# Kernel optimization log

Hardware: AMD Instinct MI355X
Metric: run time of the kernel (lower is better)

## Reference

```python
import jax, jax.numpy as jnp
import numpy as np

B, L, D_MODEL = 16, 2048, 512
S, D_LLM = 1000, 1024
H, E = 8, 64  # n_heads, d_keys
D_OUT = 64


def setup_inputs() -> dict:
    key = jax.random.key(0)
    ks = jax.random.split(key, 11)
    sc = lambda d: 1.0 / np.sqrt(d)
    return {
        "target_embedding": jax.random.normal(ks[0], (B, L, D_MODEL), dtype=jnp.float32),
        "source_embedding": jax.random.normal(ks[1], (S, D_LLM), dtype=jnp.float32),
        "value_embedding": jax.random.normal(ks[2], (S, D_LLM), dtype=jnp.float32),
        "Wq": jax.random.normal(ks[3], (D_MODEL, H * E), dtype=jnp.float32) * sc(D_MODEL),
        "bq": jnp.zeros((H * E,), dtype=jnp.float32),
        "Wk": jax.random.normal(ks[4], (D_LLM, H * E), dtype=jnp.float32) * sc(D_LLM),
        "bk": jnp.zeros((H * E,), dtype=jnp.float32),
        "Wv": jax.random.normal(ks[5], (D_LLM, H * E), dtype=jnp.float32) * sc(D_LLM),
        "bv": jnp.zeros((H * E,), dtype=jnp.float32),
        "Wo": jax.random.normal(ks[6], (H * E, D_OUT), dtype=jnp.float32) * sc(H * E),
        "bo": jnp.zeros((D_OUT,), dtype=jnp.float32),
    }


def reference(target_embedding, source_embedding, value_embedding,
              Wq, bq, Wk, bk, Wv, bv, Wo, bo):
    # projections
    q = (target_embedding @ Wq + bq).reshape(B, L, H, E)   # blhe
    k = (source_embedding @ Wk + bk).reshape(S, H, E)      # she
    v = (value_embedding @ Wv + bv).reshape(S, H, E)       # she
    scale = 1.0 / jnp.sqrt(jnp.asarray(E, dtype=q.dtype))
    scores = jnp.einsum("blhe,she->bhls", q, k)            # (B,H,L,S)
    A = jax.nn.softmax(scale * scores, axis=-1)            # dropout in eval mode = identity
    out = jnp.einsum("bhls,she->blhe", A, v).reshape(B, L, H * E)
    return out @ Wo + bo                                    # (B,L,64)
```

## Files before the change

### kernel.cpp

```cpp
#include <hip/hip_runtime.h>

typedef __attribute__((ext_vector_type(4))) float  f32x4;
typedef __attribute__((ext_vector_type(8))) __bf16 bf16x8;
typedef __attribute__((ext_vector_type(4))) __bf16 bf16x4;

static __device__ __forceinline__ f32x4 mfma16(bf16x8 a, bf16x8 b, f32x4 c) {
  return __builtin_amdgcn_mfma_f32_16x16x32_bf16(a, b, c, 0, 0, 0);
}

typedef __attribute__((address_space(1))) const unsigned int* gas1_t;
typedef __attribute__((address_space(3))) unsigned int* las3_t;
static __device__ __forceinline__ void glds16(const void* g, void* l) {
  __builtin_amdgcn_global_load_lds((gas1_t)g, (las3_t)l, 16, 0, 0);
}

#define QSCALE 0.18033688011112042f

__global__ __launch_bounds__(256) void prep_wT(
    const float* __restrict__ Wq, const float* __restrict__ Wk,
    const float* __restrict__ Wv, const float* __restrict__ Wo,
    __bf16* __restrict__ wqT, __bf16* __restrict__ wkT,
    __bf16* __restrict__ wvT, __bf16* __restrict__ woT) {
  __shared__ float tile[32][33];
  const int t = blockIdx.x;
  const float* in; __bf16* out; int K, N, tk, tn;
  if (t < 256)       { in = Wq; out = wqT; K = 512;  N = 512; tk = t & 15;          tn = t >> 4; }
  else if (t < 768)  { in = Wk; out = wkT; K = 1024; N = 512; tk = (t-256) & 31;    tn = (t-256) >> 5; }
  else if (t < 1280) { in = Wv; out = wvT; K = 1024; N = 512; tk = (t-768) & 31;    tn = (t-768) >> 5; }
  else               { in = Wo; out = woT; K = 512;  N = 64;  tk = (t-1280) & 15;   tn = (t-1280) >> 4; }
  const int k0 = tk * 32, n0 = tn * 32;
  const int c = threadIdx.x & 31, r = threadIdx.x >> 5;
#pragma unroll
  for (int i = 0; i < 4; ++i)
    tile[r + i * 8][c] = in[(size_t)(k0 + r + i * 8) * N + n0 + c];
  __syncthreads();
#pragma unroll
  for (int i = 0; i < 4; ++i)
    out[(size_t)(n0 + r + i * 8) * K + k0 + c] = (__bf16)tile[c][r + i * 8];
}

__global__ __launch_bounds__(256) void prep_cvt(
    const float* __restrict__ tgt, const float* __restrict__ src,
    const float* __restrict__ val,
    __bf16* __restrict__ tgtb, __bf16* __restrict__ srcb, __bf16* __restrict__ valb) {
  const int j = blockIdx.x * 256 + threadIdx.x;
  const int C0 = 32768 * 512 / 4;
  const int CV = 1024 * 1024 / 4;
  if (j < C0) {
    f32x4 v = *(const f32x4*)&tgt[(size_t)j * 4];
    bf16x4 o; o[0]=(__bf16)v[0]; o[1]=(__bf16)v[1]; o[2]=(__bf16)v[2]; o[3]=(__bf16)v[3];
    *(bf16x4*)&tgtb[(size_t)j * 4] = o;
  } else if (j < C0 + 2 * CV) {
    const int which = (j - C0) / CV;
    const int u = (j - C0) - which * CV;
    const float* in = which ? val : src;
    __bf16* outp = which ? valb : srcb;
    bf16x4 o;
    if (u * 4 < 1000 * 1024) {
      f32x4 v = *(const f32x4*)&in[(size_t)u * 4];
      o[0]=(__bf16)v[0]; o[1]=(__bf16)v[1]; o[2]=(__bf16)v[2]; o[3]=(__bf16)v[3];
    } else {
      o[0]=(__bf16)0.0f; o[1]=(__bf16)0.0f; o[2]=(__bf16)0.0f; o[3]=(__bf16)0.0f;
    }
    *(bf16x4*)&outp[(size_t)u * 4] = o;
  }
}

template <int MODE>
__global__ __launch_bounds__(256, 2) void gemm_bt(
    const __bf16* __restrict__ A, const __bf16* __restrict__ BT,
    const float* __restrict__ bias, float scale,
    __bf16* __restrict__ C, int M, int N, int K) {
  const int n0 = blockIdx.x * 128, m0 = blockIdx.y * 128;
  __shared__ __bf16 sA[128 * 32], sB[128 * 32];
  const int t = threadIdx.x;
  const int w = t >> 6, lane = t & 63;
  const int wr = w >> 1, wc = w & 1;
  const int lr = lane & 15, lg = lane >> 4;

  const int grow = w * 32 + (lane >> 2);
  const int lslot = (lane & 3) ^ ((lane >> 2) & 3) ^ (lane >> 4);
  char* const sAw = (char*)sA + w * 2048;
  char* const sBw = (char*)sB + w * 2048;

  const int rslot = (lg ^ (lr & 3) ^ ((lr >> 2) & 3)) << 4;
  const int aOff = wr * 4096 + lr * 64 + rslot;
  const int bOff = wc * 4096 + lr * 64 + rslot;

  f32x4 acc[4][4];
#pragma unroll
  for (int i = 0; i < 4; ++i)
#pragma unroll
    for (int j = 0; j < 4; ++j) acc[i][j] = f32x4{0.f, 0.f, 0.f, 0.f};

  const size_t gaBase0 = (size_t)(m0 + grow) * K + lslot * 8;
  const size_t gaBase1 = (size_t)(m0 + grow + 16) * K + lslot * 8;
  const size_t gbBase0 = (size_t)(n0 + grow) * K + lslot * 8;
  const size_t gbBase1 = (size_t)(n0 + grow + 16) * K + lslot * 8;

  for (int kc = 0; kc < K; kc += 32) {
    __syncthreads();
    glds16(&A[gaBase0 + kc], sAw);
    glds16(&A[gaBase1 + kc], sAw + 1024);
    glds16(&BT[gbBase0 + kc], sBw);
    glds16(&BT[gbBase1 + kc], sBw + 1024);
    __syncthreads();

    bf16x8 af[4], bfr[4];
#pragma unroll
    for (int i = 0; i < 4; ++i) {
      af[i]  = *(const bf16x8*)((const char*)sA + aOff + i * 1024);
      bfr[i] = *(const bf16x8*)((const char*)sB + bOff + i * 1024);
    }
    __builtin_amdgcn_s_setprio(1);
#pragma unroll
    for (int i = 0; i < 4; ++i)
#pragma unroll
      for (int j = 0; j < 4; ++j) acc[i][j] = mfma16(af[i], bfr[j], acc[i][j]);
    __builtin_amdgcn_s_setprio(0);
  }

#pragma unroll
  for (int i = 0; i < 4; ++i) {
    const int rowb = m0 + wr * 64 + i * 16 + lg * 4;
#pragma unroll
    for (int j = 0; j < 4; ++j) {
      const int col = n0 + wc * 64 + j * 16 + lr;
      const float bb = bias ? bias[col] : 0.0f;
      if (MODE == 0) {
#pragma unroll
        for (int r = 0; r < 4; ++r)
          C[(size_t)(rowb + r) * N + col] = (__bf16)((acc[i][j][r] + bb) * scale);
      } else {
        bf16x4 v;
#pragma unroll
        for (int r = 0; r < 4; ++r) v[r] = (__bf16)((acc[i][j][r] + bb) * scale);
        *(bf16x4*)&C[(size_t)col * M + rowb] = v;
      }
    }
  }
}

__global__ __launch_bounds__(256, 4) void attn_kernel(
    const __bf16* __restrict__ qg, const __bf16* __restrict__ kg,
    const __bf16* __restrict__ vtg, __bf16* __restrict__ og) {
  const int bid = blockIdx.x;
  const int lt = bid & 15, h = (bid >> 4) & 7, b = bid >> 7;
  const int w = threadIdx.x >> 6, lane = threadIdx.x & 63;
  const int lr = lane & 15, g = lane >> 4, lr7 = lane & 7;
  const int l0 = lt * 128 + w * 32;

  __shared__ __bf16 sK[2][4096];
  __shared__ __bf16 sV[2][4096];
  __shared__ __bf16 sP[4][1024];
  char* const pbase = (char*)&sP[w][0];

  const int srowi = lane >> 3;
  const int sslot = (lane & 7) ^ srowi;
  const int krow = w * 16 + srowi;
  const size_t kgBase = (size_t)krow * 512 + h * 64 + sslot * 8;
  const size_t vgBase = (size_t)(h * 64 + krow) * 1024 + sslot * 8;

  bf16x8 qf[2][2];
#pragma unroll
  for (int qi = 0; qi < 2; ++qi)
#pragma unroll
    for (int hf = 0; hf < 2; ++hf)
      qf[qi][hf] = *(const bf16x8*)&qg[
          ((size_t)b * 2048 + l0 + qi * 16 + lr) * 512 + h * 64 + hf * 32 + g * 8];

  f32x4 o[2][4], lsacc[2];
#pragma unroll
  for (int qi = 0; qi < 2; ++qi) {
#pragma unroll
    for (int j = 0; j < 4; ++j) o[qi][j] = f32x4{0.f, 0.f, 0.f, 0.f};
    lsacc[qi] = f32x4{0.f, 0.f, 0.f, 0.f};
  }

  bf16x8 ones8;
#pragma unroll
  for (int i = 0; i < 8; ++i) ones8[i] = (__bf16)1.0f;

  const int eOff0 = lr * 128 + ((g ^ lr7) << 4);
  const int pswz = lr7 << 4;

  glds16(&kg[kgBase], (char*)&sK[0][0] + w * 2048);
  glds16(&kg[kgBase + (size_t)8 * 512], (char*)&sK[0][0] + w * 2048 + 1024);
  glds16(&vtg[vgBase], (char*)&sV[0][0] + w * 2048);
  glds16(&vtg[vgBase + (size_t)8 * 1024], (char*)&sV[0][0] + w * 2048 + 1024);
  __syncthreads();

  for (int sc = 0; sc < 16; ++sc) {
    const int p = sc & 1;
    if (sc < 15) {
      const int sn = (sc + 1) * 64;
      char* nk = (char*)&sK[p ^ 1][0] + w * 2048;
      char* nv = (char*)&sV[p ^ 1][0] + w * 2048;
      glds16(&kg[kgBase + (size_t)sn * 512], nk);
      glds16(&kg[kgBase + (size_t)(sn + 8) * 512], nk + 1024);
      glds16(&vtg[vgBase + sn], nv);
      glds16(&vtg[vgBase + sn + 8 * 1024], nv + 1024);
    }
    const char* kbuf = (const char*)&sK[p][0];
    const char* vbuf = (const char*)&sV[p][0];

    bf16x8 kf[4][2];
#pragma unroll
    for (int t = 0; t < 4; ++t) {
      kf[t][0] = *(const bf16x8*)(kbuf + t * 2048 + eOff0);
      kf[t][1] = *(const bf16x8*)(kbuf + t * 2048 + (eOff0 ^ 64));
    }
    f32x4 d[2][4];
    __builtin_amdgcn_s_setprio(1);
#pragma unroll
    for (int qi = 0; qi < 2; ++qi)
#pragma unroll
      for (int t = 0; t < 4; ++t) {
        f32x4 z = {0.f, 0.f, 0.f, 0.f};
        z = mfma16(kf[t][0], qf[qi][0], z);
        z = mfma16(kf[t][1], qf[qi][1], z);
        d[qi][t] = z;
      }
    __builtin_amdgcn_s_setprio(0);
    if (sc == 15) {
#pragma unroll
      for (int qi = 0; qi < 2; ++qi)
#pragma unroll
        for (int t = 0; t < 4; ++t)
#pragma unroll
          for (int r = 0; r < 4; ++r)
            if (960 + t * 16 + 4 * g + r >= 1000) d[qi][t][r] = -1.0e30f;
    }

    bf16x8 vf[2][4];
#pragma unroll
    for (int kc = 0; kc < 2; ++kc)
#pragma unroll
      for (int j = 0; j < 4; ++j)
        vf[kc][j] = *(const bf16x8*)(vbuf + j * 2048 + (eOff0 ^ (kc * 64)));

#pragma unroll
    for (int qi = 0; qi < 2; ++qi) {
#pragma unroll
      for (int t = 0; t < 4; ++t) {
        bf16x4 pv;
        pv[0] = (__bf16)exp2f(d[qi][t][0]);
        pv[1] = (__bf16)exp2f(d[qi][t][1]);
        pv[2] = (__bf16)exp2f(d[qi][t][2]);
        pv[3] = (__bf16)exp2f(d[qi][t][3]);
        *(bf16x4*)(pbase + lr * 128 + ((t * 32 + g * 8) ^ pswz)) = pv;
      }
#pragma unroll
      for (int kc = 0; kc < 2; ++kc) {
        const bf16x8 pB = *(const bf16x8*)(
            pbase + lr * 128 + ((kc * 64 + g * 16) ^ pswz));
        __builtin_amdgcn_s_setprio(1);
        lsacc[qi] = mfma16(ones8, pB, lsacc[qi]);
#pragma unroll
        for (int j = 0; j < 4; ++j)
          o[qi][j] = mfma16(vf[kc][j], pB, o[qi][j]);
        __builtin_amdgcn_s_setprio(0);
      }
    }
    __syncthreads();
  }

#pragma unroll
  for (int qi = 0; qi < 2; ++qi) {
    const float rinv = 1.0f / lsacc[qi][0];
    const size_t rowb = ((size_t)b * 2048 + l0 + qi * 16 + lr) * 512 + h * 64;
#pragma unroll
    for (int j = 0; j < 4; ++j) {
      bf16x4 v;
#pragma unroll
      for (int r = 0; r < 4; ++r) v[r] = (__bf16)(o[qi][j][r] * rinv);
      *(bf16x4*)&og[rowb + j * 16 + 4 * g] = v;
    }
  }
}

__global__ __launch_bounds__(256) void out_proj(
    const __bf16* __restrict__ ab, const __bf16* __restrict__ woT,
    const float* __restrict__ bo, float* __restrict__ out) {
  const int w = threadIdx.x >> 6, lane = threadIdx.x & 63;
  const int lr = lane & 15, g = lane >> 4;
  const int r0 = blockIdx.x * 64 + w * 16;
  f32x4 acc[4];
#pragma unroll
  for (int j = 0; j < 4; ++j) acc[j] = f32x4{0.f, 0.f, 0.f, 0.f};
  for (int kc = 0; kc < 512; kc += 32) {
    const bf16x8 af = *(const bf16x8*)&ab[(size_t)(r0 + lr) * 512 + kc + g * 8];
#pragma unroll
    for (int j = 0; j < 4; ++j) {
      const bf16x8 bf = *(const bf16x8*)&woT[(size_t)(j * 16 + lr) * 512 + kc + g * 8];
      acc[j] = mfma16(af, bf, acc[j]);
    }
  }
#pragma unroll
  for (int j = 0; j < 4; ++j) {
    const int col = j * 16 + lr;
    const float bb = bo[col];
#pragma unroll
    for (int r = 0; r < 4; ++r)
      out[(size_t)(r0 + 4 * g + r) * 64 + col] = acc[j][r] + bb;
  }
}

extern "C" void kernel_launch(void* const* d_in, const int* in_sizes, int n_in,
                              void* d_out, int out_size, void* d_ws, size_t ws_size,
                              hipStream_t stream) {
  const float* tgt = (const float*)d_in[0];
  const float* src = (const float*)d_in[1];
  const float* val = (const float*)d_in[2];
  const float* Wq  = (const float*)d_in[3];
  const float* bq  = (const float*)d_in[4];
  const float* Wk  = (const float*)d_in[5];
  const float* bk  = (const float*)d_in[6];
  const float* Wv  = (const float*)d_in[7];
  const float* bv  = (const float*)d_in[8];
  const float* Wo  = (const float*)d_in[9];
  const float* bo  = (const float*)d_in[10];
  float* out = (float*)d_out;
  char* ws = (char*)d_ws;

  __bf16* wqT  = (__bf16*)(ws + 0);
  __bf16* wkT  = (__bf16*)(ws + 524288);
  __bf16* wvT  = (__bf16*)(ws + 1572864);
  __bf16* woT  = (__bf16*)(ws + 2621440);
  __bf16* srcb = (__bf16*)(ws + 2686976);
  __bf16* valb = (__bf16*)(ws + 4784128);
  __bf16* kb   = (__bf16*)(ws + 6881280);
  __bf16* vtb  = (__bf16*)(ws + 7929856);
  __bf16* tgtb = (__bf16*)(ws + 8978432);
  __bf16* attnb= (__bf16*)(ws + 8978432);
  __bf16* qb   = (__bf16*)(ws + 42532864);

  prep_wT<<<1312, 256, 0, stream>>>(Wq, Wk, Wv, Wo, wqT, wkT, wvT, woT);
  prep_cvt<<<18432, 256, 0, stream>>>(tgt, src, val, tgtb, srcb, valb);

  gemm_bt<0><<<dim3(4, 256), 256, 0, stream>>>(tgtb, wqT, bq, QSCALE, qb, 32768, 512, 512);
  gemm_bt<0><<<dim3(4, 8), 256, 0, stream>>>(srcb, wkT, bk, 1.0f, kb, 1024, 512, 1024);
  gemm_bt<1><<<dim3(4, 8), 256, 0, stream>>>(valb, wvT, bv, 1.0f, vtb, 1024, 512, 1024);

  attn_kernel<<<2048, 256, 0, stream>>>(qb, kb, vtb, attnb);

  out_proj<<<512, 256, 0, stream>>>(attnb, woT, bo, out);
}
```

Before: 361.0 us.

## Double-buffer GEMM LDS tiles and stage attention output through LDS

The projection GEMM now keeps two LDS buffers, loading the next K-chunk while MFMAs run on the current one, which removes one barrier per iteration. The attention epilogue writes the normalized output into the per-wave LDS scratch, then reads it back so each lane issues full 16-byte row-contiguous global stores instead of scattered 8-byte ones. Shared memory for the GEMM doubles, which may reduce occupancy. Reusing the P scratch also depends on per-wave ownership and on the swizzle matching.

```diff
diff --git a/kernel.cpp b/kernel.cpp
--- a/kernel.cpp
+++ b/kernel.cpp
@@ -72,7 +72,7 @@
     const float* __restrict__ bias, float scale,
     __bf16* __restrict__ C, int M, int N, int K) {
   const int n0 = blockIdx.x * 128, m0 = blockIdx.y * 128;
-  __shared__ __bf16 sA[128 * 32], sB[128 * 32];
+  __shared__ __bf16 sA[2][128 * 32], sB[2][128 * 32];
   const int t = threadIdx.x;
   const int w = t >> 6, lane = t & 63;
   const int wr = w >> 1, wc = w & 1;
@@ -80,8 +80,7 @@
 
   const int grow = w * 32 + (lane >> 2);
   const int lslot = (lane & 3) ^ ((lane >> 2) & 3) ^ (lane >> 4);
-  char* const sAw = (char*)sA + w * 2048;
-  char* const sBw = (char*)sB + w * 2048;
+  const int woff = w * 2048;
 
   const int rslot = (lg ^ (lr & 3) ^ ((lr >> 2) & 3)) << 4;
   const int aOff = wr * 4096 + lr * 64 + rslot;
@@ -98,19 +97,27 @@
   const size_t gbBase0 = (size_t)(n0 + grow) * K + lslot * 8;
   const size_t gbBase1 = (size_t)(n0 + grow + 16) * K + lslot * 8;
 
-  for (int kc = 0; kc < K; kc += 32) {
-    __syncthreads();
-    glds16(&A[gaBase0 + kc], sAw);
-    glds16(&A[gaBase1 + kc], sAw + 1024);
-    glds16(&BT[gbBase0 + kc], sBw);
-    glds16(&BT[gbBase1 + kc], sBw + 1024);
-    __syncthreads();
-
+  glds16(&A[gaBase0], (char*)sA[0] + woff);
+  glds16(&A[gaBase1], (char*)sA[0] + woff + 1024);
+  glds16(&BT[gbBase0], (char*)sB[0] + woff);
+  glds16(&BT[gbBase1], (char*)sB[0] + woff + 1024);
+  __syncthreads();
+
+  const int NK = K >> 5;
+  for (int it = 0; it < NK; ++it) {
+    const int cur = it & 1;
+    if (it + 1 < NK) {
+      const int kc = (it + 1) << 5;
+      glds16(&A[gaBase0 + kc], (char*)sA[cur ^ 1] + woff);
+      glds16(&A[gaBase1 + kc], (char*)sA[cur ^ 1] + woff + 1024);
+      glds16(&BT[gbBase0 + kc], (char*)sB[cur ^ 1] + woff);
+      glds16(&BT[gbBase1 + kc], (char*)sB[cur ^ 1] + woff + 1024);
+    }
     bf16x8 af[4], bfr[4];
 #pragma unroll
     for (int i = 0; i < 4; ++i) {
-      af[i]  = *(const bf16x8*)((const char*)sA + aOff + i * 1024);
-      bfr[i] = *(const bf16x8*)((const char*)sB + bOff + i * 1024);
+      af[i]  = *(const bf16x8*)((const char*)sA[cur] + aOff + i * 1024);
+      bfr[i] = *(const bf16x8*)((const char*)sB[cur] + bOff + i * 1024);
     }
     __builtin_amdgcn_s_setprio(1);
 #pragma unroll
@@ -118,6 +125,7 @@
 #pragma unroll
       for (int j = 0; j < 4; ++j) acc[i][j] = mfma16(af[i], bfr[j], acc[i][j]);
     __builtin_amdgcn_s_setprio(0);
+    __syncthreads();
   }
 
 #pragma unroll
@@ -265,17 +273,23 @@
     __syncthreads();
   }
 
+  const int rr = lane >> 2, cc = lane & 3;
+  const int rsw = (rr & 7) << 4;
 #pragma unroll
   for (int qi = 0; qi < 2; ++qi) {
     const float rinv = 1.0f / lsacc[qi][0];
-    const size_t rowb = ((size_t)b * 2048 + l0 + qi * 16 + lr) * 512 + h * 64;
 #pragma unroll
     for (int j = 0; j < 4; ++j) {
       bf16x4 v;
 #pragma unroll
       for (int r = 0; r < 4; ++r) v[r] = (__bf16)(o[qi][j][r] * rinv);
-      *(bf16x4*)&og[rowb + j * 16 + 4 * g] = v;
-    }
+      *(bf16x4*)(pbase + lr * 128 + ((j * 32 + g * 8) ^ pswz)) = v;
+    }
+    const uint4 lo = *(const uint4*)(pbase + rr * 128 + ((cc * 16) ^ rsw));
+    const uint4 hi = *(const uint4*)(pbase + rr * 128 + ((cc * 16 + 64) ^ rsw));
+    char* orow = (char*)&og[((size_t)b * 2048 + l0 + qi * 16 + rr) * 512 + h * 64];
+    *(uint4*)(orow + cc * 16) = lo;
+    *(uint4*)(orow + cc * 16 + 64) = hi;
   }
 }
 
```

After: 362.6 us. No clear change (+0.4%).
